# Kernel optimization log

Measured on AMD Instinct MI355X. Metric: run time of the kernel, lower is better.

The kernel has to match this reference:

```python
import jax, jax.numpy as jnp
import numpy as np

N = 100000      # nodes
E = 1600000     # edges (avg degree 16)
IN = 128        # in_size
H = 4           # num_heads
DH = 16         # hid_size (per-head)
DO = 16         # out_size (per-head)
NEG_SLOPE = 0.2 # DGL GATConv default leaky_relu slope


def setup_inputs():
    key = jax.random.key(0)
    ks = jax.random.split(key, 12)
    s = 0.1
    return {
        "x":   jax.random.normal(ks[0], (N, IN), jnp.float32),
        "src": jax.random.randint(ks[1], (E,), 0, N, jnp.int32),
        "dst": jax.random.randint(ks[2], (E,), 0, N, jnp.int32),
        # layer 1: in=128 -> H*DH=64, residual Linear (128 != 64)
        "W1":    jax.random.normal(ks[3], (IN, H * DH), jnp.float32) * s,
        "al1":   jax.random.normal(ks[4], (H, DH), jnp.float32) * s,
        "ar1":   jax.random.normal(ks[5], (H, DH), jnp.float32) * s,
        "resW1": jax.random.normal(ks[6], (IN, H * DH), jnp.float32) * s,
        "b1":    jnp.zeros((H * DH,), jnp.float32),
        # layer 2: in=H*DH=64 -> H*DO=64, residual is Identity reshape (64 == 64)
        "W2":  jax.random.normal(ks[7], (H * DH, H * DO), jnp.float32) * s,
        "al2": jax.random.normal(ks[8], (H, DO), jnp.float32) * s,
        "ar2": jax.random.normal(ks[9], (H, DO), jnp.float32) * s,
        "b2":  jnp.zeros((H * DO,), jnp.float32),
    }


def gat_layer(h, W, al, ar, res, bias, src, dst):
    """One DGL-style GATConv (no internal activation). Returns [N, H, D]."""
    d = W.shape[1] // H
    feat = (h @ W).reshape(-1, H, d)                       # [N,H,D]
    el = jnp.einsum('nhd,hd->nh', feat, al)                # [N,H]
    er = jnp.einsum('nhd,hd->nh', feat, ar)                # [N,H]
    e = jax.nn.leaky_relu(el[src] + er[dst], NEG_SLOPE)    # [E,H]
    # segment softmax over incoming edges of each destination node
    emax = jax.lax.stop_gradient(jax.ops.segment_max(e, dst, num_segments=N))
    ee = jnp.exp(e - emax[dst])                            # [E,H]
    den = jax.ops.segment_sum(ee, dst, num_segments=N)     # [N,H]
    alpha = ee / den[dst]                                  # [E,H]
    msg = alpha[:, :, None] * feat[src]                    # [E,H,D]
    out = jax.ops.segment_sum(msg, dst, num_segments=N)    # [N,H,D]
    return out + res + bias.reshape(1, H, d)


def reference(x, src, dst, W1, al1, ar1, resW1, b1, W2, al2, ar2, b2):
    # layer 1 (residual via Linear since IN != H*DH)
    res1 = (x @ resW1).reshape(N, H, DH)
    h = gat_layer(x, W1, al1, ar1, res1, b1, src, dst)     # [N,H,DH]
    h = jax.nn.elu(h.reshape(N, H * DH))                   # flatten + elu (dropout=eval identity)
    # layer 2 (identity residual since H*DH == H*DO)
    res2 = h.reshape(N, H, DO)
    h = gat_layer(h, W2, al2, ar2, res2, b2, src, dst)     # [N,H,DO]
    return h.mean(axis=1)                                  # [N,DO]
```

## Files before the change

### kernel.cpp

```cpp
#include <hip/hip_runtime.h>
#include <hip/hip_bf16.h>

static inline int cdiv(int a, int b){ return (a+b-1)/b; }

#define LEAKY(x) ((x) >= 0.f ? (x) : 0.2f*(x))

#define NBK   512
#define NBKSH 9
#define CAP   12288

__device__ inline unsigned short bf16bits(float f){
  __hip_bfloat16 h = __float2bfloat16(f);
  return *reinterpret_cast<unsigned short*>(&h);
}


__global__ __launch_bounds__(256) void binA(const int* __restrict__ src,
    const int* __restrict__ dst, int* __restrict__ acur, unsigned int* __restrict__ tmp,
    int E, int B, int epb)
{
  __shared__ int cnt1[256], cnt2[256], gbase[256];
  const int tid = threadIdx.x;
  cnt1[tid] = 0; cnt2[tid] = 0;
  __syncthreads();
  const int beg = blockIdx.x*epb, end = min(E, beg+epb);
  for (int e = beg+tid; e < end; e += 256) atomicAdd(&cnt1[dst[e]>>NBKSH], 1);
  __syncthreads();
  if (tid < B) gbase[tid] = atomicAdd(&acur[tid], cnt1[tid]);
  __syncthreads();
  for (int e = beg+tid; e < end; e += 256) {
    int s = src[e], d = dst[e];
    int b = d >> NBKSH;
    int tk = atomicAdd(&cnt2[b], 1);
    int slot = gbase[b] + tk;
    if (slot < CAP)
      tmp[(size_t)b*CAP + slot] = ((unsigned)s << NBKSH) | (unsigned)(d & (NBK-1));
  }
}


__global__ __launch_bounds__(256) void bucket_scan(const int* __restrict__ acur,
    int* __restrict__ bbase, int* __restrict__ off, int B, int N, int E)
{
  __shared__ int wsum[4];
  const int tid = threadIdx.x, lane = tid & 63, wave = tid >> 6;
  int v = (tid < B) ? acur[tid] : 0;
  int x = v;
  #pragma unroll
  for (int s = 1; s < 64; s <<= 1) { int t = __shfl_up(x, s); if (lane >= s) x += t; }
  if (lane == 63) wsum[wave] = x;
  __syncthreads();
  if (tid == 0) { int r = 0; for (int w = 0; w < 4; w++) { int t = wsum[w]; wsum[w] = r; r += t; } }
  __syncthreads();
  int excl = wsum[wave] + x - v;
  if (tid < B)    bbase[tid] = excl;
  if (tid == B-1) bbase[B]   = excl + v;
  if (tid == 0)   off[N]     = E;
}


__global__ __launch_bounds__(256) void binC(const unsigned int* __restrict__ tmp,
    const int* __restrict__ acur, const int* __restrict__ bbase,
    int* __restrict__ off, int* __restrict__ csr_src, int N)
{
  __shared__ int sA[NBK], sB[NBK];
  const int b = blockIdx.x, tid = threadIdx.x;
  const int m = min(acur[b], CAP);
  const int base = bbase[b];
  const int n0 = b*NBK;
  const int nn = min(NBK, N - n0);
  for (int j = tid; j < NBK; j += 256) sA[j] = 0;
  __syncthreads();
  const unsigned int* tb = tmp + (size_t)b*CAP;
  for (int i = tid; i < m; i += 256) atomicAdd(&sA[tb[i] & (NBK-1)], 1);
  __syncthreads();
  int* in = sA; int* ob = sB;
  for (int st = 1; st < NBK; st <<= 1) {
    for (int j = tid; j < NBK; j += 256) { int v = in[j]; if (j >= st) v += in[j-st]; ob[j] = v; }
    __syncthreads();
    int* t = in; in = ob; ob = t;
  }
  for (int j = tid; j < NBK; j += 256) ob[j] = j ? in[j-1] : 0;
  __syncthreads();
  for (int j = tid; j < nn; j += 256) off[n0 + j] = base + ob[j];
  __syncthreads();
  for (int i = tid; i < m; i += 256) {
    unsigned v = tb[i];
    int pos = atomicAdd(&ob[v & (NBK-1)], 1);
    csr_src[base + pos] = (int)(v >> NBKSH);
  }
}


template<bool ATTN, bool BF16OUT>
__global__ __launch_bounds__(256) void lin128(const float* __restrict__ X,
    const float* __restrict__ W, const float* __restrict__ al, const float* __restrict__ ar,
    void* __restrict__ featout, float* __restrict__ el, float* __restrict__ er, int n)
{
  __shared__ float Ws[128*64];
  __shared__ float Xs[32*129];
  const int tid = threadIdx.x;
  const int nbase = blockIdx.x * 32;
  for (int i = tid; i < 128*64/4; i += 256) ((float4*)Ws)[i] = ((const float4*)W)[i];
  for (int idx = tid; idx < 32*32; idx += 256) {
    int node = idx >> 5, fq = idx & 31;
    int gn = nbase + node;
    float4 v = (gn < n) ? ((const float4*)X)[(size_t)gn*32 + fq] : float4{0.f,0.f,0.f,0.f};
    Xs[node*129 + fq*4 + 0] = v.x;
    Xs[node*129 + fq*4 + 1] = v.y;
    Xs[node*129 + fq*4 + 2] = v.z;
    Xs[node*129 + fq*4 + 3] = v.w;
  }
  __syncthreads();
  const int c0 = (tid & 15) * 4;
  const int n0 = (tid >> 4) * 2;
  float a00=0,a01=0,a02=0,a03=0, a10=0,a11=0,a12=0,a13=0;
  #pragma unroll 4
  for (int k = 0; k < 128; k++) {
    float4 w = *(const float4*)&Ws[k*64 + c0];
    float x0 = Xs[n0*129 + k];
    float x1 = Xs[n0*129 + 129 + k];
    a00 = fmaf(x0, w.x, a00); a01 = fmaf(x0, w.y, a01);
    a02 = fmaf(x0, w.z, a02); a03 = fmaf(x0, w.w, a03);
    a10 = fmaf(x1, w.x, a10); a11 = fmaf(x1, w.y, a11);
    a12 = fmaf(x1, w.z, a12); a13 = fmaf(x1, w.w, a13);
  }
  const int g0 = nbase + n0, g1 = g0 + 1;
  if (BF16OUT) {
    unsigned short* fb = (unsigned short*)featout;
    if (g0 < n) *(ushort4*)&fb[(size_t)g0*64 + c0] = ushort4{bf16bits(a00),bf16bits(a01),bf16bits(a02),bf16bits(a03)};
    if (g1 < n) *(ushort4*)&fb[(size_t)g1*64 + c0] = ushort4{bf16bits(a10),bf16bits(a11),bf16bits(a12),bf16bits(a13)};
  } else {
    float* fb = (float*)featout;
    if (g0 < n) *(float4*)&fb[(size_t)g0*64 + c0] = float4{a00,a01,a02,a03};
    if (g1 < n) *(float4*)&fb[(size_t)g1*64 + c0] = float4{a10,a11,a12,a13};
  }
  if (ATTN) {
    float l0=al[c0], l1=al[c0+1], l2=al[c0+2], l3=al[c0+3];
    float r0=ar[c0], r1=ar[c0+1], r2=ar[c0+2], r3=ar[c0+3];
    float e0 = a00*l0 + a01*l1 + a02*l2 + a03*l3;
    float e1 = a10*l0 + a11*l1 + a12*l2 + a13*l3;
    float q0 = a00*r0 + a01*r1 + a02*r2 + a03*r3;
    float q1 = a10*r0 + a11*r1 + a12*r2 + a13*r3;
    e0 += __shfl_xor(e0,1); e0 += __shfl_xor(e0,2);
    e1 += __shfl_xor(e1,1); e1 += __shfl_xor(e1,2);
    q0 += __shfl_xor(q0,1); q0 += __shfl_xor(q0,2);
    q1 += __shfl_xor(q1,1); q1 += __shfl_xor(q1,2);
    if ((tid & 3) == 0) {
      int h = (tid & 15) >> 2;
      if (g0 < n) { el[g0*4+h] = e0; er[g0*4+h] = q0; }
      if (g1 < n) { el[g1*4+h] = e1; er[g1*4+h] = q1; }
    }
  }
}


__global__ __launch_bounds__(256) void lin64(const float* __restrict__ X,
    const float* __restrict__ W, const float* __restrict__ al, const float* __restrict__ ar,
    unsigned short* __restrict__ feat, float* __restrict__ el, float* __restrict__ er, int n)
{
  __shared__ float Ws[64*64];
  __shared__ float Xs[64*65];
  const int tid = threadIdx.x;
  const int nbase = blockIdx.x * 64;
  for (int i = tid; i < 64*64/4; i += 256) ((float4*)Ws)[i] = ((const float4*)W)[i];
  for (int idx = tid; idx < 64*16; idx += 256) {
    int node = idx >> 4, fq = idx & 15;
    int gn = nbase + node;
    float4 v = (gn < n) ? ((const float4*)X)[(size_t)gn*16 + fq] : float4{0.f,0.f,0.f,0.f};
    Xs[node*65 + fq*4 + 0] = v.x;
    Xs[node*65 + fq*4 + 1] = v.y;
    Xs[node*65 + fq*4 + 2] = v.z;
    Xs[node*65 + fq*4 + 3] = v.w;
  }
  __syncthreads();
  const int c0 = (tid & 15) * 4;
  const int n0 = (tid >> 4) * 4;
  float acc[4][4];
  #pragma unroll
  for (int i = 0; i < 4; i++)
    #pragma unroll
    for (int j = 0; j < 4; j++) acc[i][j] = 0.f;
  #pragma unroll 4
  for (int k = 0; k < 64; k++) {
    float4 w = *(const float4*)&Ws[k*64 + c0];
    #pragma unroll
    for (int i = 0; i < 4; i++) {
      float x = Xs[(n0+i)*65 + k];
      acc[i][0] = fmaf(x, w.x, acc[i][0]);
      acc[i][1] = fmaf(x, w.y, acc[i][1]);
      acc[i][2] = fmaf(x, w.z, acc[i][2]);
      acc[i][3] = fmaf(x, w.w, acc[i][3]);
    }
  }
  float l0=al[c0], l1=al[c0+1], l2=al[c0+2], l3=al[c0+3];
  float r0=ar[c0], r1=ar[c0+1], r2=ar[c0+2], r3=ar[c0+3];
  #pragma unroll
  for (int i = 0; i < 4; i++) {
    int g = nbase + n0 + i;
    if (g < n) *(ushort4*)&feat[(size_t)g*64 + c0] =
        ushort4{bf16bits(acc[i][0]),bf16bits(acc[i][1]),bf16bits(acc[i][2]),bf16bits(acc[i][3])};
    float e = acc[i][0]*l0 + acc[i][1]*l1 + acc[i][2]*l2 + acc[i][3]*l3;
    float q = acc[i][0]*r0 + acc[i][1]*r1 + acc[i][2]*r2 + acc[i][3]*r3;
    e += __shfl_xor(e,1); e += __shfl_xor(e,2);
    q += __shfl_xor(q,1); q += __shfl_xor(q,2);
    if ((tid & 3) == 0 && g < n) {
      int h = (tid & 15) >> 2;
      el[g*4+h] = e; er[g*4+h] = q;
    }
  }
}


template<int LAYER>
__global__ __launch_bounds__(256) void aggregate_fused(const int* __restrict__ off,
    const int* __restrict__ csr_src, const float* __restrict__ el, const float* __restrict__ er,
    const __hip_bfloat16* __restrict__ feat, const float* __restrict__ res,
    const float* __restrict__ bias, float* __restrict__ out, int n)
{
  const int wave = threadIdx.x >> 6, lane = threadIdx.x & 63;
  const int node = blockIdx.x*4 + wave;
  if (node >= n) return;
  const int h = lane >> 4;
  const float erh = er[node*4 + h];
  const int beg = off[node], end = off[node+1];
  float d[8], a[8];
  #pragma unroll
  for (int k = 0; k < 8; k++) { d[k] = 0.f; a[k] = 0.f; }
  int i = beg;
  for (; i + 8 <= end; i += 8) {
    int   s[8]; float p[8], f[8];
    #pragma unroll
    for (int k = 0; k < 8; k++) s[k] = csr_src[i+k];
    #pragma unroll
    for (int k = 0; k < 8; k++) p[k] = __expf(LEAKY(el[s[k]*4 + h] + erh));
    #pragma unroll
    for (int k = 0; k < 8; k++) f[k] = __bfloat162float(feat[(size_t)s[k]*64 + lane]);
    #pragma unroll
    for (int k = 0; k < 8; k++) { d[k] += p[k]; a[k] = fmaf(p[k], f[k], a[k]); }
  }
  for (; i < end; i++) {
    int s = csr_src[i];
    float p = __expf(LEAKY(el[s*4 + h] + erh));
    d[0] += p;
    a[0] = fmaf(p, __bfloat162float(feat[(size_t)s*64 + lane]), a[0]);
  }
  float den = ((d[0]+d[1])+(d[2]+d[3])) + ((d[4]+d[5])+(d[6]+d[7]));
  float acc = ((a[0]+a[1])+(a[2]+a[3])) + ((a[4]+a[5])+(a[6]+a[7]));
  float v = (den > 0.f) ? (acc/den) : 0.f;
  v += res[(size_t)node*64 + lane] + bias[lane];
  if (LAYER == 1) {
    v = (v > 0.f) ? v : expm1f(v);
    out[(size_t)node*64 + lane] = v;
  } else {
    v += __shfl_xor(v, 16);
    v += __shfl_xor(v, 32);
    if (lane < 16) out[(size_t)node*16 + lane] = 0.25f*v;
  }
}


extern "C" void kernel_launch(void* const* d_in, const int* in_sizes, int n_in,
                              void* d_out, int out_size, void* d_ws, size_t ws_size,
                              hipStream_t stream)
{
  (void)n_in; (void)out_size; (void)ws_size;
  const float* x   = (const float*)d_in[0];
  const int*   src = (const int*)  d_in[1];
  const int*   dst = (const int*)  d_in[2];
  const float* W1  = (const float*)d_in[3];
  const float* al1 = (const float*)d_in[4];
  const float* ar1 = (const float*)d_in[5];
  const float* rW1 = (const float*)d_in[6];
  const float* b1  = (const float*)d_in[7];
  const float* W2  = (const float*)d_in[8];
  const float* al2 = (const float*)d_in[9];
  const float* ar2 = (const float*)d_in[10];
  const float* b2  = (const float*)d_in[11];
  float* out = (float*)d_out;

  const int N_ = in_sizes[0] / 128;
  const int E_ = in_sizes[1];
  const int B_ = cdiv(N_, NBK);

  char* ws = (char*)d_ws;
  size_t o = 0;
  auto alloc = [&](size_t bytes)->char* {
    char* p = ws + o; o += (bytes + 255) & ~(size_t)255; return p;
  };
  int*   acur    = (int*)  alloc((size_t)B_*4);
  int*   bbase   = (int*)  alloc(((size_t)B_+1)*4);
  int*   off     = (int*)  alloc(((size_t)N_+1)*4);
  unsigned int* tmp = (unsigned int*)alloc((size_t)B_*CAP*4);
  int*   csr_src = (int*)  alloc((size_t)E_*4);
  unsigned short* featb = (unsigned short*)alloc((size_t)N_*64*2);
  float* el      = (float*)alloc((size_t)N_*4*4);
  float* er      = (float*)alloc((size_t)N_*4*4);
  float* hbuf    = (float*)alloc((size_t)N_*64*4);

  hipMemsetAsync(acur, 0, (size_t)B_*4, stream);
  binA<<<256, 256, 0, stream>>>(src, dst, acur, tmp, E_, B_, cdiv(E_,256));
  bucket_scan<<<1, 256, 0, stream>>>(acur, bbase, off, B_, N_, E_);
  binC<<<B_, 256, 0, stream>>>(tmp, acur, bbase, off, csr_src, N_);

  lin128<true,  true ><<<cdiv(N_,32), 256, 0, stream>>>(x, W1,  al1, ar1, featb, el, er, N_);
  lin128<false, false><<<cdiv(N_,32), 256, 0, stream>>>(x, rW1, nullptr, nullptr, hbuf, nullptr, nullptr, N_);
  aggregate_fused<1><<<cdiv(N_,4), 256, 0, stream>>>(off, csr_src, el, er,
      (const __hip_bfloat16*)featb, hbuf, b1, hbuf, N_);

  lin64<<<cdiv(N_,64), 256, 0, stream>>>(hbuf, W2, al2, ar2, featb, el, er, N_);
  aggregate_fused<2><<<cdiv(N_,4), 256, 0, stream>>>(off, csr_src, el, er,
      (const __hip_bfloat16*)featb, hbuf, b2, out, N_);
}
```

Before: 444.6 us.

## Fuse layer-1 linears, shrink CSR buckets, precompute edge exps in shared memory

Three separate changes. The two 128-wide linear kernels become one that loads x once and reuses it for both the W1 and residual weights, removing a second full read of x. The binning bucket size drops from 512 to 256 nodes, giving more bucket blocks with smaller capacity. The aggregation kernel now computes the exp attention weights for a block's edges cooperatively into shared memory with float4 el loads, instead of each lane doing a scalar gather and exp per head; this adds a barrier, up to 16KB of shared memory per block, and an unrolled-free fallback path for blocks with many edges.

```diff
diff --git a/kernel.cpp b/kernel.cpp
--- a/kernel.cpp
+++ b/kernel.cpp
@@ -5,9 +5,10 @@
 
 #define LEAKY(x) ((x) >= 0.f ? (x) : 0.2f*(x))
 
-#define NBK   512
-#define NBKSH 9
-#define CAP   12288
+#define NBK   256
+#define NBKSH 8
+#define CAP   5120
+#define SCAP  1024
 
 __device__ inline unsigned short bf16bits(float f){
   __hip_bfloat16 h = __float2bfloat16(f);
@@ -19,14 +20,14 @@
     const int* __restrict__ dst, int* __restrict__ acur, unsigned int* __restrict__ tmp,
     int E, int B, int epb)
 {
-  __shared__ int cnt1[256], cnt2[256], gbase[256];
+  __shared__ int cnt1[512], cnt2[512], gbase[512];
   const int tid = threadIdx.x;
-  cnt1[tid] = 0; cnt2[tid] = 0;
+  for (int j = tid; j < 512; j += 256) { cnt1[j] = 0; cnt2[j] = 0; }
   __syncthreads();
   const int beg = blockIdx.x*epb, end = min(E, beg+epb);
   for (int e = beg+tid; e < end; e += 256) atomicAdd(&cnt1[dst[e]>>NBKSH], 1);
   __syncthreads();
-  if (tid < B) gbase[tid] = atomicAdd(&acur[tid], cnt1[tid]);
+  for (int j = tid; j < B; j += 256) gbase[j] = atomicAdd(&acur[j], cnt1[j]);
   __syncthreads();
   for (int e = beg+tid; e < end; e += 256) {
     int s = src[e], d = dst[e];
@@ -39,10 +40,10 @@
 }
 
 
-__global__ __launch_bounds__(256) void bucket_scan(const int* __restrict__ acur,
+__global__ __launch_bounds__(512) void bucket_scan(const int* __restrict__ acur,
     int* __restrict__ bbase, int* __restrict__ off, int B, int N, int E)
 {
-  __shared__ int wsum[4];
+  __shared__ int wsum[8];
   const int tid = threadIdx.x, lane = tid & 63, wave = tid >> 6;
   int v = (tid < B) ? acur[tid] : 0;
   int x = v;
@@ -50,7 +51,7 @@
   for (int s = 1; s < 64; s <<= 1) { int t = __shfl_up(x, s); if (lane >= s) x += t; }
   if (lane == 63) wsum[wave] = x;
   __syncthreads();
-  if (tid == 0) { int r = 0; for (int w = 0; w < 4; w++) { int t = wsum[w]; wsum[w] = r; r += t; } }
+  if (tid == 0) { int r = 0; for (int w = 0; w < 8; w++) { int t = wsum[w]; wsum[w] = r; r += t; } }
   __syncthreads();
   int excl = wsum[wave] + x - v;
   if (tid < B)    bbase[tid] = excl;
@@ -69,20 +70,20 @@
   const int base = bbase[b];
   const int n0 = b*NBK;
   const int nn = min(NBK, N - n0);
-  for (int j = tid; j < NBK; j += 256) sA[j] = 0;
+  if (tid < NBK) sA[tid] = 0;
   __syncthreads();
   const unsigned int* tb = tmp + (size_t)b*CAP;
   for (int i = tid; i < m; i += 256) atomicAdd(&sA[tb[i] & (NBK-1)], 1);
   __syncthreads();
   int* in = sA; int* ob = sB;
   for (int st = 1; st < NBK; st <<= 1) {
-    for (int j = tid; j < NBK; j += 256) { int v = in[j]; if (j >= st) v += in[j-st]; ob[j] = v; }
+    if (tid < NBK) { int v = in[tid]; if (tid >= st) v += in[tid-st]; ob[tid] = v; }
     __syncthreads();
     int* t = in; in = ob; ob = t;
   }
-  for (int j = tid; j < NBK; j += 256) ob[j] = j ? in[j-1] : 0;
-  __syncthreads();
-  for (int j = tid; j < nn; j += 256) off[n0 + j] = base + ob[j];
+  if (tid < NBK) ob[tid] = tid ? in[tid-1] : 0;
+  __syncthreads();
+  if (tid < nn) off[n0 + tid] = base + ob[tid];
   __syncthreads();
   for (int i = tid; i < m; i += 256) {
     unsigned v = tb[i];
@@ -92,10 +93,11 @@
 }
 
 
-template<bool ATTN, bool BF16OUT>
-__global__ __launch_bounds__(256) void lin128(const float* __restrict__ X,
-    const float* __restrict__ W, const float* __restrict__ al, const float* __restrict__ ar,
-    void* __restrict__ featout, float* __restrict__ el, float* __restrict__ er, int n)
+__global__ __launch_bounds__(256) void lin128_once(const float* __restrict__ X,
+    const float* __restrict__ W, const float* __restrict__ RW,
+    const float* __restrict__ al, const float* __restrict__ ar,
+    unsigned short* __restrict__ featb, float* __restrict__ el, float* __restrict__ er,
+    float* __restrict__ res, int n)
 {
   __shared__ float Ws[128*64];
   __shared__ float Xs[32*129];
@@ -114,28 +116,21 @@
   __syncthreads();
   const int c0 = (tid & 15) * 4;
   const int n0 = (tid >> 4) * 2;
-  float a00=0,a01=0,a02=0,a03=0, a10=0,a11=0,a12=0,a13=0;
-  #pragma unroll 4
-  for (int k = 0; k < 128; k++) {
-    float4 w = *(const float4*)&Ws[k*64 + c0];
-    float x0 = Xs[n0*129 + k];
-    float x1 = Xs[n0*129 + 129 + k];
-    a00 = fmaf(x0, w.x, a00); a01 = fmaf(x0, w.y, a01);
-    a02 = fmaf(x0, w.z, a02); a03 = fmaf(x0, w.w, a03);
-    a10 = fmaf(x1, w.x, a10); a11 = fmaf(x1, w.y, a11);
-    a12 = fmaf(x1, w.z, a12); a13 = fmaf(x1, w.w, a13);
-  }
   const int g0 = nbase + n0, g1 = g0 + 1;
-  if (BF16OUT) {
-    unsigned short* fb = (unsigned short*)featout;
-    if (g0 < n) *(ushort4*)&fb[(size_t)g0*64 + c0] = ushort4{bf16bits(a00),bf16bits(a01),bf16bits(a02),bf16bits(a03)};
-    if (g1 < n) *(ushort4*)&fb[(size_t)g1*64 + c0] = ushort4{bf16bits(a10),bf16bits(a11),bf16bits(a12),bf16bits(a13)};
-  } else {
-    float* fb = (float*)featout;
-    if (g0 < n) *(float4*)&fb[(size_t)g0*64 + c0] = float4{a00,a01,a02,a03};
-    if (g1 < n) *(float4*)&fb[(size_t)g1*64 + c0] = float4{a10,a11,a12,a13};
-  }
-  if (ATTN) {
+  {
+    float a00=0,a01=0,a02=0,a03=0, a10=0,a11=0,a12=0,a13=0;
+    #pragma unroll 4
+    for (int k = 0; k < 128; k++) {
+      float4 w = *(const float4*)&Ws[k*64 + c0];
+      float x0 = Xs[n0*129 + k];
+      float x1 = Xs[n0*129 + 129 + k];
+      a00 = fmaf(x0, w.x, a00); a01 = fmaf(x0, w.y, a01);
+      a02 = fmaf(x0, w.z, a02); a03 = fmaf(x0, w.w, a03);
+      a10 = fmaf(x1, w.x, a10); a11 = fmaf(x1, w.y, a11);
+      a12 = fmaf(x1, w.z, a12); a13 = fmaf(x1, w.w, a13);
+    }
+    if (g0 < n) *(ushort4*)&featb[(size_t)g0*64 + c0] = ushort4{bf16bits(a00),bf16bits(a01),bf16bits(a02),bf16bits(a03)};
+    if (g1 < n) *(ushort4*)&featb[(size_t)g1*64 + c0] = ushort4{bf16bits(a10),bf16bits(a11),bf16bits(a12),bf16bits(a13)};
     float l0=al[c0], l1=al[c0+1], l2=al[c0+2], l3=al[c0+3];
     float r0=ar[c0], r1=ar[c0+1], r2=ar[c0+2], r3=ar[c0+3];
     float e0 = a00*l0 + a01*l1 + a02*l2 + a03*l3;
@@ -151,6 +146,24 @@
       if (g0 < n) { el[g0*4+h] = e0; er[g0*4+h] = q0; }
       if (g1 < n) { el[g1*4+h] = e1; er[g1*4+h] = q1; }
     }
+  }
+  __syncthreads();
+  for (int i = tid; i < 128*64/4; i += 256) ((float4*)Ws)[i] = ((const float4*)RW)[i];
+  __syncthreads();
+  {
+    float a00=0,a01=0,a02=0,a03=0, a10=0,a11=0,a12=0,a13=0;
+    #pragma unroll 4
+    for (int k = 0; k < 128; k++) {
+      float4 w = *(const float4*)&Ws[k*64 + c0];
+      float x0 = Xs[n0*129 + k];
+      float x1 = Xs[n0*129 + 129 + k];
+      a00 = fmaf(x0, w.x, a00); a01 = fmaf(x0, w.y, a01);
+      a02 = fmaf(x0, w.z, a02); a03 = fmaf(x0, w.w, a03);
+      a10 = fmaf(x1, w.x, a10); a11 = fmaf(x1, w.y, a11);
+      a12 = fmaf(x1, w.z, a12); a13 = fmaf(x1, w.w, a13);
+    }
+    if (g0 < n) *(float4*)&res[(size_t)g0*64 + c0] = float4{a00,a01,a02,a03};
+    if (g1 < n) *(float4*)&res[(size_t)g1*64 + c0] = float4{a10,a11,a12,a13};
   }
 }
 
@@ -218,32 +231,69 @@
     const __hip_bfloat16* __restrict__ feat, const float* __restrict__ res,
     const float* __restrict__ bias, float* __restrict__ out, int n)
 {
-  const int wave = threadIdx.x >> 6, lane = threadIdx.x & 63;
-  const int node = blockIdx.x*4 + wave;
+  __shared__ float sp[SCAP*4];
+  __shared__ float er_s[4][4];
+  __shared__ int   so[5];
+  const int tid = threadIdx.x, wave = tid >> 6, lane = tid & 63;
+  const int nb = blockIdx.x*4;
+  if (tid < 5) so[tid] = off[min(nb + tid, n)];
+  if (tid >= 5 && tid < 21) {
+    int t = tid - 5;
+    int g = nb + (t >> 2);
+    er_s[t >> 2][t & 3] = (g < n) ? er[g*4 + (t & 3)] : 0.f;
+  }
+  __syncthreads();
+  const int b0 = so[0], b4 = so[4];
+  const int cnt = b4 - b0;
+  const bool staged = cnt <= SCAP;
+  if (staged) {
+    const int o1 = so[1], o2 = so[2], o3 = so[3];
+    for (int j = b0 + tid; j < b4; j += 256) {
+      int s = csr_src[j];
+      int t = (j >= o1) + (j >= o2) + (j >= o3);
+      float4 l = *(const float4*)&el[s*4];
+      int li = j - b0;
+      sp[li*4+0] = __expf(LEAKY(l.x + er_s[t][0]));
+      sp[li*4+1] = __expf(LEAKY(l.y + er_s[t][1]));
+      sp[li*4+2] = __expf(LEAKY(l.z + er_s[t][2]));
+      sp[li*4+3] = __expf(LEAKY(l.w + er_s[t][3]));
+    }
+  }
+  __syncthreads();
+  const int node = nb + wave;
   if (node >= n) return;
   const int h = lane >> 4;
-  const float erh = er[node*4 + h];
-  const int beg = off[node], end = off[node+1];
+  const int beg = so[wave], end = so[wave+1];
   float d[8], a[8];
   #pragma unroll
   for (int k = 0; k < 8; k++) { d[k] = 0.f; a[k] = 0.f; }
   int i = beg;
-  for (; i + 8 <= end; i += 8) {
-    int   s[8]; float p[8], f[8];
-    #pragma unroll
-    for (int k = 0; k < 8; k++) s[k] = csr_src[i+k];
-    #pragma unroll
-    for (int k = 0; k < 8; k++) p[k] = __expf(LEAKY(el[s[k]*4 + h] + erh));
-    #pragma unroll
-    for (int k = 0; k < 8; k++) f[k] = __bfloat162float(feat[(size_t)s[k]*64 + lane]);
-    #pragma unroll
-    for (int k = 0; k < 8; k++) { d[k] += p[k]; a[k] = fmaf(p[k], f[k], a[k]); }
-  }
-  for (; i < end; i++) {
-    int s = csr_src[i];
-    float p = __expf(LEAKY(el[s*4 + h] + erh));
-    d[0] += p;
-    a[0] = fmaf(p, __bfloat162float(feat[(size_t)s*64 + lane]), a[0]);
+  if (staged) {
+    for (; i + 8 <= end; i += 8) {
+      int   s[8]; float p[8], f[8];
+      #pragma unroll
+      for (int k = 0; k < 8; k++) s[k] = csr_src[i+k];
+      #pragma unroll
+      for (int k = 0; k < 8; k++) p[k] = sp[(i+k-b0)*4 + h];
+      #pragma unroll
+      for (int k = 0; k < 8; k++) f[k] = __bfloat162float(feat[(size_t)s[k]*64 + lane]);
+      #pragma unroll
+      for (int k = 0; k < 8; k++) { d[k] += p[k]; a[k] = fmaf(p[k], f[k], a[k]); }
+    }
+    for (; i < end; i++) {
+      int s = csr_src[i];
+      float p = sp[(i-b0)*4 + h];
+      d[0] += p;
+      a[0] = fmaf(p, __bfloat162float(feat[(size_t)s*64 + lane]), a[0]);
+    }
+  } else {
+    const float erh = er_s[wave][h];
+    for (; i < end; i++) {
+      int s = csr_src[i];
+      float p = __expf(LEAKY(el[s*4 + h] + erh));
+      d[0] += p;
+      a[0] = fmaf(p, __bfloat162float(feat[(size_t)s*64 + lane]), a[0]);
+    }
   }
   float den = ((d[0]+d[1])+(d[2]+d[3])) + ((d[4]+d[5])+(d[6]+d[7]));
   float acc = ((a[0]+a[1])+(a[2]+a[3])) + ((a[4]+a[5])+(a[6]+a[7]));
@@ -300,11 +350,10 @@
 
   hipMemsetAsync(acur, 0, (size_t)B_*4, stream);
   binA<<<256, 256, 0, stream>>>(src, dst, acur, tmp, E_, B_, cdiv(E_,256));
-  bucket_scan<<<1, 256, 0, stream>>>(acur, bbase, off, B_, N_, E_);
+  bucket_scan<<<1, 512, 0, stream>>>(acur, bbase, off, B_, N_, E_);
   binC<<<B_, 256, 0, stream>>>(tmp, acur, bbase, off, csr_src, N_);
 
-  lin128<true,  true ><<<cdiv(N_,32), 256, 0, stream>>>(x, W1,  al1, ar1, featb, el, er, N_);
-  lin128<false, false><<<cdiv(N_,32), 256, 0, stream>>>(x, rW1, nullptr, nullptr, hbuf, nullptr, nullptr, N_);
+  lin128_once<<<cdiv(N_,32), 256, 0, stream>>>(x, W1, rW1, al1, ar1, featb, el, er, hbuf, N_);
   aggregate_fused<1><<<cdiv(N_,4), 256, 0, stream>>>(off, csr_src, el, er,
       (const __hip_bfloat16*)featb, hbuf, b1, hbuf, N_);
 
```

Result: faster. 406.8 us (-8.5%).
